# Optimization experiments

Measured on AMD Instinct MI355X. Metric: run time of the kernel, lower is better.

Reference implementation:

```python
import jax, jax.numpy as jnp
import numpy as np

B, T, C, H, E, TOPK, DR = 2, 2048, 768, 3072, 8, 2, 24


def setup_inputs() -> dict:
    key = jax.random.key(0)
    ks = jax.random.split(key, 16)
    std = 0.02
    n = lambda k, shape, s=std: (s * jax.random.normal(k, shape)).astype(jnp.float32)
    emb = jax.random.normal(ks[3], (E, DR), dtype=jnp.float32)
    emb = emb / (jnp.linalg.norm(emb, axis=-1, keepdims=True) + 1e-8)
    return {
        "x": jax.random.normal(ks[0], (B, T, C), dtype=jnp.float32),
        "router_w": n(ks[1], (E, C)),
        "probe_w": n(ks[2], (DR, C)),
        "router_emb": emb,
        "fatigue": jnp.zeros((E,), jnp.float32),
        "energy": jnp.ones((E,), jnp.float32),
        "w_fast1": n(ks[4], (E, C, H)),
        "w_slow1": n(ks[5], (E, C, H)),
        "h_fast1": n(ks[6], (E, C, H), 0.005),
        "m_gate1": jax.random.uniform(ks[7], (E,), dtype=jnp.float32),
        "b1": jnp.zeros((E, H), jnp.float32),
        "w_fast2": n(ks[8], (E, H, C)),
        "w_slow2": n(ks[9], (E, H, C)),
        "h_fast2": n(ks[10], (E, H, C), 0.005),
        "m_gate2": jax.random.uniform(ks[11], (E,), dtype=jnp.float32),
        "b2": jnp.zeros((E, C), jnp.float32),
    }


def _normalize(v, axis=-1, eps=1e-12):
    # matches F.normalize: v / max(||v||, eps)
    return v / jnp.maximum(jnp.linalg.norm(v, axis=axis, keepdims=True), eps)


def reference(x, router_w, probe_w, router_emb, fatigue, energy,
              w_fast1, w_slow1, h_fast1, m_gate1, b1,
              w_fast2, w_slow2, h_fast2, m_gate2, b2):
    Bd, Td, Cd = x.shape
    # --- router logits with biology-inspired biases ---
    logits = jnp.einsum('btc,ec->bte', x, router_w)            # nn.Linear, no bias
    tok_proxy = x.mean(axis=-1, keepdims=True)                  # [B,T,1]
    router_gain = jnp.linalg.norm(router_emb, axis=-1)          # [E]
    base_bias = 0.02 * tok_proxy                                # broadcasts over E
    gain_bias = 0.02 * tok_proxy * router_gain                  # [B,T,E]
    tok_unit = _normalize(jnp.einsum('btc,dc->btd', x, probe_w))
    align_bias = 0.02 * jnp.einsum('btd,ed->bte', tok_unit, _normalize(router_emb))
    logits = logits + base_bias + gain_bias + align_bias + 0.1 * energy - 0.1 * fatigue
    # --- top-k gating ---
    g, idx = jax.lax.top_k(logits, TOPK)                        # [B,T,K]
    gates = jax.nn.softmax(g, axis=-1)
    N = Bd * Td
    gates_full = jnp.zeros((N, E), x.dtype).at[
        jnp.arange(N)[:, None], idx.reshape(N, TOPK)].set(gates.reshape(N, TOPK))
    flat_x = x.reshape(N, Cd)
    # --- expert dispatch: dynamic W = w_fast + m_gate*w_slow + H_fast ---
    def body(acc, p):
        wf1, ws1, hf1, mg1, bb1, wf2, ws2, hf2, mg2, bb2, ge = p
        W1 = wf1 + mg1 * ws1 + hf1                              # [C,H]
        h = jnp.square(jnp.maximum(flat_x @ W1 + bb1, 0.0))     # relu(y)^2
        W2 = wf2 + mg2 * ws2 + hf2                              # [H,C]
        y = h @ W2 + bb2
        return acc + ge[:, None] * y, None
    out, _ = jax.lax.scan(
        body, jnp.zeros((N, Cd), x.dtype),
        (w_fast1, w_slow1, h_fast1, m_gate1, b1,
         w_fast2, w_slow2, h_fast2, m_gate2, b2, gates_full.T))
    return out.reshape(Bd, Td, Cd)
```

## Files before the change

kernel.cpp:

```cpp
#include <hip/hip_runtime.h>

typedef unsigned short u16;
typedef __attribute__((ext_vector_type(8))) short short8;
typedef __attribute__((ext_vector_type(8))) unsigned short ushort8;
typedef __attribute__((ext_vector_type(4))) unsigned short ushort4v;
typedef __attribute__((ext_vector_type(4))) float f32x4;

static constexpr int Cdim = 768;
static constexpr int Hdim = 3072;
static constexpr int Edim = 8;
static constexpr int Ntok = 4096;
static constexpr int DRc  = 24;
static constexpr int NSLOT = Ntok * 2;
static constexpr int NCHUNK = 8;
static constexpr int CCH = Cdim / NCHUNK;
static constexpr int KS2 = 3;
static constexpr int KC2 = Hdim / KS2;
static constexpr int MAXROWS = 71;

static constexpr size_t OFF_XB   = 0;
static constexpr size_t OFF_W1T  = 6291456;
static constexpr size_t OFF_W2T  = 44040192;
static constexpr size_t OFF_HBUF = 81788928;
static constexpr size_t OFF_XT   = OFF_HBUF;
static constexpr size_t OFF_PART = OFF_HBUF + 12582912;
static constexpr size_t OFF_YB   = OFF_W1T;
static constexpr size_t OFF_TOK  = 132120576;
static constexpr size_t OFF_RM   = 132251648;
static constexpr size_t OFF_NR   = 132252160;
static constexpr size_t OFF_CNT  = 132382720;
static constexpr size_t OFF_OFFS = 132382752;
static constexpr size_t OFF_TSLOT= 132382784;
static constexpr size_t OFF_TG   = 132448320;

__device__ __forceinline__ u16 f2bf(float f) {
  unsigned u = __builtin_bit_cast(unsigned, f);
  u += 0x7fffu + ((u >> 16) & 1u);
  return (u16)(u >> 16);
}

__device__ __forceinline__ float bf2f(u16 v) {
  unsigned u = ((unsigned)v) << 16;
  return __builtin_bit_cast(float, u);
}

__device__ __forceinline__ void gld16(const u16* g, u16* l) {
  __builtin_amdgcn_global_load_lds((const __attribute__((address_space(1))) unsigned int*)g,
                                   (__attribute__((address_space(3))) unsigned int*)l,
                                   16, 0, 0);
}

__device__ __forceinline__ int xcd_remap(int p, int nwg) {
  int q = nwg >> 3, rem = nwg & 7;
  int x = p & 7, i = p >> 3;
  return (x < rem ? x * (q + 1) : rem * (q + 1) + (x - rem) * q) + i;
}

__global__ __launch_bounds__(256)
void prep_x2_kernel(const float* __restrict__ x, u16* __restrict__ x16,
                    float* __restrict__ xT) {
  __shared__ float tile[64][65];
  const int c0 = blockIdx.x * 64;
  const int t0 = blockIdx.y * 64;
  const int tid = threadIdx.x;
  const int row = tid >> 4, col = (tid & 15) * 4;
  #pragma unroll
  for (int i = 0; i < 4; i++) {
    int r = row + i * 16;
    size_t idx = (size_t)(t0 + r) * Cdim + c0 + col;
    float4 v = *(const float4*)(x + idx);
    tile[r][col + 0] = v.x; tile[r][col + 1] = v.y;
    tile[r][col + 2] = v.z; tile[r][col + 3] = v.w;
    ushort4v o = { f2bf(v.x), f2bf(v.y), f2bf(v.z), f2bf(v.w) };
    *reinterpret_cast<ushort4v*>(x16 + idx) = o;
  }
  __syncthreads();
  const int c = tid >> 2, tg = (tid & 3) * 16;
  #pragma unroll
  for (int q = 0; q < 4; q++) {
    float4 w;
    w.x = tile[tg + q * 4 + 0][c];
    w.y = tile[tg + q * 4 + 1][c];
    w.z = tile[tg + q * 4 + 2][c];
    w.w = tile[tg + q * 4 + 3][c];
    *reinterpret_cast<float4*>(xT + (size_t)(c0 + c) * Ntok + t0 + tg + q * 4) = w;
  }
}

__global__ __launch_bounds__(256)
void prep_wt_kernel(const float* __restrict__ wf, const float* __restrict__ wsl,
                    const float* __restrict__ hf, const float* __restrict__ mg,
                    u16* __restrict__ outw, const int R, const int Ccol) {
  __shared__ u16 tileT[64][66];
  const int e = blockIdx.z;
  const int r0 = blockIdx.x * 64, c0 = blockIdx.y * 64;
  const float m = mg[e];
  const size_t base = (size_t)e * R * Ccol;
  const int t = threadIdx.x;
  const int cr = t >> 4, cc = (t & 15) * 4;
  #pragma unroll
  for (int i = 0; i < 4; i++) {
    int r = cr + i * 16;
    size_t idx = base + (size_t)(r0 + r) * Ccol + (c0 + cc);
    float4 a = *(const float4*)(wf + idx);
    float4 b = *(const float4*)(wsl + idx);
    float4 h = *(const float4*)(hf + idx);
    tileT[cc + 0][r] = f2bf(fmaf(m, b.x, a.x) + h.x);
    tileT[cc + 1][r] = f2bf(fmaf(m, b.y, a.y) + h.y);
    tileT[cc + 2][r] = f2bf(fmaf(m, b.z, a.z) + h.z);
    tileT[cc + 3][r] = f2bf(fmaf(m, b.w, a.w) + h.w);
  }
  __syncthreads();
  const int oc = t >> 2, ch = (t & 3) * 16;
  ushort8 o0, o1;
  #pragma unroll
  for (int j = 0; j < 8; j++) { o0[j] = tileT[oc][ch + j]; o1[j] = tileT[oc][ch + 8 + j]; }
  size_t oidx = ((size_t)e * Ccol + c0 + oc) * R + r0 + ch;
  *reinterpret_cast<ushort8*>(outw + oidx) = o0;
  *reinterpret_cast<ushort8*>(outw + oidx + 8) = o1;
}

__global__ __launch_bounds__(256)
void logits_part_kernel(const float* __restrict__ xT, const float* __restrict__ router_w,
                        const float* __restrict__ probe_w, float* __restrict__ part) {
  const int t = blockIdx.x * 256 + threadIdx.x;
  const int cB = blockIdx.y * CCH;
  float racc[Edim] = {};
  float pacc[DRc] = {};
  float sacc = 0.f;
  for (int ci = 0; ci < CCH; ci++) {
    int c = cB + ci;
    float xv = xT[(size_t)c * Ntok + t];
    sacc += xv;
    #pragma unroll
    for (int ee = 0; ee < Edim; ee++) racc[ee] = fmaf(xv, router_w[ee * Cdim + c], racc[ee]);
    #pragma unroll
    for (int d = 0; d < DRc; d++) pacc[d] = fmaf(xv, probe_w[d * Cdim + c], pacc[d]);
  }
  float* pb = part + (size_t)blockIdx.y * 33 * Ntok + t;
  #pragma unroll
  for (int ee = 0; ee < Edim; ee++) pb[(size_t)ee * Ntok] = racc[ee];
  #pragma unroll
  for (int d = 0; d < DRc; d++) pb[(size_t)(8 + d) * Ntok] = pacc[d];
  pb[(size_t)32 * Ntok] = sacc;
}

__global__ __launch_bounds__(256)
void router_fin_kernel(const float* __restrict__ part, const float* __restrict__ emb,
                       const float* __restrict__ fatigue, const float* __restrict__ energy,
                       int* __restrict__ counts, int* __restrict__ tok_list,
                       int4* __restrict__ tokslot, float2* __restrict__ tokgate) {
  const int t = blockIdx.x * 256 + threadIdx.x;
  float v[33];
  #pragma unroll
  for (int o = 0; o < 33; o++) {
    float s = 0.f;
    #pragma unroll
    for (int ch = 0; ch < NCHUNK; ch++)
      s += part[((size_t)ch * 33 + o) * Ntok + t];
    v[o] = s;
  }
  const float* racc = v;
  const float* pacc = v + 8;
  float proxy = v[32] / 768.f;
  float pn2 = 0.f;
  #pragma unroll
  for (int d = 0; d < DRc; d++) pn2 += pacc[d] * pacc[d];
  float pnorm = sqrtf(pn2);
  float logitv[Edim];
  #pragma unroll
  for (int ee = 0; ee < Edim; ee++) {
    float g2 = 0.f, dote = 0.f;
    #pragma unroll
    for (int d = 0; d < DRc; d++) {
      float ev = emb[ee * DRc + d];
      g2 += ev * ev;
      dote += pacc[d] * ev;
    }
    float gain = sqrtf(g2);
    float align = dote / (fmaxf(pnorm, 1e-12f) * fmaxf(gain, 1e-12f));
    logitv[ee] = racc[ee] + 0.02f * proxy * (1.f + gain) + 0.02f * align
               + 0.1f * energy[ee] - 0.1f * fatigue[ee];
  }
  int e0 = 0; float b0v = logitv[0];
  #pragma unroll
  for (int ee = 1; ee < Edim; ee++) if (logitv[ee] > b0v) { b0v = logitv[ee]; e0 = ee; }
  int e1 = -1; float b1v = -3.4e38f;
  #pragma unroll
  for (int ee = 0; ee < Edim; ee++) if (ee != e0 && logitv[ee] > b1v) { b1v = logitv[ee]; e1 = ee; }
  float texp = expf(b1v - b0v);
  float g0 = 1.f / (1.f + texp);
  float g1 = texp / (1.f + texp);
  int p0 = atomicAdd(&counts[e0], 1);
  tok_list[e0 * Ntok + p0] = t;
  int p1 = atomicAdd(&counts[e1], 1);
  tok_list[e1 * Ntok + p1] = t;
  tokslot[t] = make_int4(e0, p0, e1, p1);
  tokgate[t] = make_float2(g0, g1);
}

__global__ void offsets_kernel(const int* __restrict__ counts, int* __restrict__ offs,
                               int* __restrict__ rowmap, int* __restrict__ nrows) {
  if (threadIdx.x == 0) {
    int r = 0, nr = 0;
    for (int e = 0; e < Edim; e++) {
      offs[e] = r;
      int ne = counts[e];
      for (int tb = 0; tb < ne; tb += 128) rowmap[nr++] = (e << 16) | (tb >> 7);
      r += ne;
    }
    nrows[0] = nr;
  }
}

__global__ __launch_bounds__(256)
void fc1_kernel(const u16* __restrict__ x16, const u16* __restrict__ W1T,
                const float* __restrict__ b1, const int* __restrict__ counts,
                const int* __restrict__ offs, const int* __restrict__ tok_list,
                const int* __restrict__ rowmap, const int* __restrict__ nrows,
                u16* __restrict__ h_buf) {
  const int l = xcd_remap(blockIdx.x, MAXROWS * 24);
  const int r = l / 24;
  if (r >= nrows[0]) return;
  const int hB = l % 24;
  const int rm = rowmap[r];
  const int e = rm >> 16;
  const int tokBase = (rm & 0xffff) << 7;
  const int n_e = counts[e];
  const int hBase = hB * 128;
  __shared__ u16 As[2][4096];
  __shared__ u16 Bs[2][4096];
  __shared__ int toks[128];
  const int tid = threadIdx.x;
  if (tid < 128) {
    int s = tokBase + tid;
    toks[tid] = (s < n_e) ? tok_list[e * Ntok + s] : 0;
  }
  __syncthreads();
  const int lane = tid & 63, wv = tid >> 6;
  const int wr = wv >> 1, wc = wv & 1;
  const int sRow = lane >> 2, sSlot = lane & 3;
  const int kbOff = (sSlot ^ ((sRow >> 1) & 3)) * 8;
  const int rA0 = wv * 16 + sRow, rA1 = 64 + rA0;
  const u16* pA0 = x16 + (size_t)toks[rA0] * Cdim + kbOff;
  const u16* pA1 = x16 + (size_t)toks[rA1] * Cdim + kbOff;
  const u16* pB0 = W1T + ((size_t)e * Hdim + hBase + rA0) * Cdim + kbOff;
  const u16* pB1 = W1T + ((size_t)e * Hdim + hBase + rA1) * Cdim + kbOff;
  const int stOff = wv * 512 + lane * 8;
  const int fr = lane & 15;
  const int qsw = (((lane >> 4) ^ ((fr >> 1) & 3))) * 8;
  f32x4 acc[4][4] = {};
  gld16(pA0, &As[0][stOff]);
  gld16(pA1, &As[0][2048 + stOff]);
  gld16(pB0, &Bs[0][stOff]);
  gld16(pB1, &Bs[0][2048 + stOff]);
  __syncthreads();
  int cur = 0;
  for (int it = 0; it < 24; it++) {
    if (it < 23) {
      int k1 = (it + 1) * 32;
      gld16(pA0 + k1, &As[cur ^ 1][stOff]);
      gld16(pA1 + k1, &As[cur ^ 1][2048 + stOff]);
      gld16(pB0 + k1, &Bs[cur ^ 1][stOff]);
      gld16(pB1 + k1, &Bs[cur ^ 1][2048 + stOff]);
    }
    short8 aF[4], bF[4];
    #pragma unroll
    for (int m = 0; m < 4; m++)
      aF[m] = *reinterpret_cast<const short8*>(&As[cur][(wr * 64 + m * 16 + fr) * 32 + qsw]);
    #pragma unroll
    for (int n = 0; n < 4; n++)
      bF[n] = *reinterpret_cast<const short8*>(&Bs[cur][(wc * 64 + n * 16 + fr) * 32 + qsw]);
    #pragma unroll
    for (int m = 0; m < 4; m++)
      #pragma unroll
      for (int n = 0; n < 4; n++)
        acc[m][n] = __builtin_amdgcn_mfma_f32_16x16x32_bf16(aF[m], bF[n], acc[m][n], 0, 0, 0);
    __syncthreads();
    cur ^= 1;
  }
  const int rq = (lane >> 4) * 4;
  float bias[4];
  #pragma unroll
  for (int n = 0; n < 4; n++) bias[n] = b1[(size_t)e * Hdim + hBase + wc * 64 + n * 16 + fr];
  const int rowB = offs[e] + tokBase;
  #pragma unroll
  for (int m = 0; m < 4; m++) {
    #pragma unroll
    for (int j = 0; j < 4; j++) {
      int rl = wr * 64 + m * 16 + rq + j;
      if (tokBase + rl < n_e) {
        size_t rb = (size_t)(rowB + rl) * Hdim + hBase + wc * 64 + fr;
        #pragma unroll
        for (int n = 0; n < 4; n++) {
          float v = fmaxf(acc[m][n][j] + bias[n], 0.f);
          h_buf[rb + n * 16] = f2bf(v * v);
        }
      }
    }
  }
}

__global__ __launch_bounds__(256)
void fc2_kernel(const u16* __restrict__ h_buf, const u16* __restrict__ W2T,
                const float* __restrict__ b2, const int* __restrict__ counts,
                const int* __restrict__ offs, const int* __restrict__ rowmap,
                const int* __restrict__ nrows, u16* __restrict__ ybuf) {
  const int l = xcd_remap(blockIdx.x, MAXROWS * 18);
  const int r = l / 18;
  if (r >= nrows[0]) return;
  const int xb = l % 18;
  const int rm = rowmap[r];
  const int e = rm >> 16;
  const int tokBase = (rm & 0xffff) << 7;
  const int n_e = counts[e];
  const int kch = xb / 6;
  const int cBase = (xb % 6) * 128;
  const size_t kOff = (size_t)kch * KC2;
  __shared__ u16 As[2][4096];
  __shared__ u16 Bs[2][4096];
  const int tid = threadIdx.x;
  const int lane = tid & 63, wv = tid >> 6;
  const int wr = wv >> 1, wc = wv & 1;
  const int sRow = lane >> 2, sSlot = lane & 3;
  const int kbOff = (sSlot ^ ((sRow >> 1) & 3)) * 8;
  const int rA0 = wv * 16 + sRow, rA1 = 64 + rA0;
  const int slotB = offs[e] + tokBase;
  const int s0 = min(slotB + rA0, NSLOT - 1);
  const int s1 = min(slotB + rA1, NSLOT - 1);
  const u16* pA0 = h_buf + (size_t)s0 * Hdim + kOff + kbOff;
  const u16* pA1 = h_buf + (size_t)s1 * Hdim + kOff + kbOff;
  const u16* pB0 = W2T + ((size_t)e * Cdim + cBase + rA0) * Hdim + kOff + kbOff;
  const u16* pB1 = W2T + ((size_t)e * Cdim + cBase + rA1) * Hdim + kOff + kbOff;
  const int stOff = wv * 512 + lane * 8;
  const int fr = lane & 15;
  const int qsw = (((lane >> 4) ^ ((fr >> 1) & 3))) * 8;
  f32x4 acc[4][4] = {};
  gld16(pA0, &As[0][stOff]);
  gld16(pA1, &As[0][2048 + stOff]);
  gld16(pB0, &Bs[0][stOff]);
  gld16(pB1, &Bs[0][2048 + stOff]);
  __syncthreads();
  int cur = 0;
  for (int it = 0; it < KC2 / 32; it++) {
    if (it < KC2 / 32 - 1) {
      int k1 = (it + 1) * 32;
      gld16(pA0 + k1, &As[cur ^ 1][stOff]);
      gld16(pA1 + k1, &As[cur ^ 1][2048 + stOff]);
      gld16(pB0 + k1, &Bs[cur ^ 1][stOff]);
      gld16(pB1 + k1, &Bs[cur ^ 1][2048 + stOff]);
    }
    short8 aF[4], bF[4];
    #pragma unroll
    for (int m = 0; m < 4; m++)
      aF[m] = *reinterpret_cast<const short8*>(&As[cur][(wr * 64 + m * 16 + fr) * 32 + qsw]);
    #pragma unroll
    for (int n = 0; n < 4; n++)
      bF[n] = *reinterpret_cast<const short8*>(&Bs[cur][(wc * 64 + n * 16 + fr) * 32 + qsw]);
    #pragma unroll
    for (int m = 0; m < 4; m++)
      #pragma unroll
      for (int n = 0; n < 4; n++)
        acc[m][n] = __builtin_amdgcn_mfma_f32_16x16x32_bf16(aF[m], bF[n], acc[m][n], 0, 0, 0);
    __syncthreads();
    cur ^= 1;
  }
  const int rq = (lane >> 4) * 4;
  float bias[4];
  #pragma unroll
  for (int n = 0; n < 4; n++)
    bias[n] = (kch == 0) ? b2[(size_t)e * Cdim + cBase + wc * 64 + n * 16 + fr] : 0.f;
  u16* yb = ybuf + (size_t)kch * NSLOT * Cdim;
  #pragma unroll
  for (int m = 0; m < 4; m++) {
    #pragma unroll
    for (int j = 0; j < 4; j++) {
      int rl = wr * 64 + m * 16 + rq + j;
      if (tokBase + rl < n_e) {
        u16* ob = yb + (size_t)(slotB + rl) * Cdim + cBase + wc * 64 + fr;
        #pragma unroll
        for (int n = 0; n < 4; n++)
          ob[n * 16] = f2bf(acc[m][n][j] + bias[n]);
      }
    }
  }
}

__global__ __launch_bounds__(256)
void gather_kernel(const u16* __restrict__ ybuf, const int4* __restrict__ tokslot,
                   const float2* __restrict__ tokgate, const int* __restrict__ offs,
                   float* __restrict__ out) {
  const int gid = blockIdx.x * 256 + threadIdx.x;
  const int t = gid / 192;
  const int c4 = (gid - t * 192) * 4;
  int4 ts = tokslot[t];
  float2 g = tokgate[t];
  size_t s0 = (size_t)(offs[ts.x] + ts.y) * Cdim + c4;
  size_t s1 = (size_t)(offs[ts.z] + ts.w) * Cdim + c4;
  const size_t K1 = (size_t)NSLOT * Cdim;
  float acc0[4] = {}, acc1[4] = {};
  #pragma unroll
  for (int k = 0; k < KS2; k++) {
    ushort4v a = *reinterpret_cast<const ushort4v*>(ybuf + k * K1 + s0);
    ushort4v b = *reinterpret_cast<const ushort4v*>(ybuf + k * K1 + s1);
    #pragma unroll
    for (int j = 0; j < 4; j++) { acc0[j] += bf2f(a[j]); acc1[j] += bf2f(b[j]); }
  }
  float4 o;
  o.x = g.x * acc0[0] + g.y * acc1[0];
  o.y = g.x * acc0[1] + g.y * acc1[1];
  o.z = g.x * acc0[2] + g.y * acc1[2];
  o.w = g.x * acc0[3] + g.y * acc1[3];
  *reinterpret_cast<float4*>(out + (size_t)t * Cdim + c4) = o;
}

extern "C" void kernel_launch(void* const* d_in, const int* in_sizes, int n_in,
                              void* d_out, int out_size, void* d_ws, size_t ws_size,
                              hipStream_t stream) {
  const float* x        = (const float*)d_in[0];
  const float* router_w = (const float*)d_in[1];
  const float* probe_w  = (const float*)d_in[2];
  const float* emb      = (const float*)d_in[3];
  const float* fatigue  = (const float*)d_in[4];
  const float* energy   = (const float*)d_in[5];
  const float* wf1      = (const float*)d_in[6];
  const float* ws1      = (const float*)d_in[7];
  const float* hf1      = (const float*)d_in[8];
  const float* mg1      = (const float*)d_in[9];
  const float* b1       = (const float*)d_in[10];
  const float* wf2      = (const float*)d_in[11];
  const float* ws2      = (const float*)d_in[12];
  const float* hf2      = (const float*)d_in[13];
  const float* mg2      = (const float*)d_in[14];
  const float* b2       = (const float*)d_in[15];
  float* out = (float*)d_out;
  char* ws = (char*)d_ws;

  u16*    x16       = (u16*)(ws + OFF_XB);
  u16*    W1T       = (u16*)(ws + OFF_W1T);
  u16*    W2T       = (u16*)(ws + OFF_W2T);
  u16*    hbuf      = (u16*)(ws + OFF_HBUF);
  float*  xT        = (float*)(ws + OFF_XT);
  float*  part      = (float*)(ws + OFF_PART);
  u16*    ybuf      = (u16*)(ws + OFF_YB);
  int*    tok_list  = (int*)(ws + OFF_TOK);
  int*    rowmap    = (int*)(ws + OFF_RM);
  int*    nrows     = (int*)(ws + OFF_NR);
  int*    counts    = (int*)(ws + OFF_CNT);
  int*    offs      = (int*)(ws + OFF_OFFS);
  int4*   tokslot   = (int4*)(ws + OFF_TSLOT);
  float2* tokgate   = (float2*)(ws + OFF_TG);

  hipMemsetAsync(counts, 0, 64, stream);

  prep_x2_kernel<<<dim3(Cdim / 64, Ntok / 64), 256, 0, stream>>>(x, x16, xT);
  logits_part_kernel<<<dim3(Ntok / 256, NCHUNK), 256, 0, stream>>>(xT, router_w, probe_w, part);
  router_fin_kernel<<<Ntok / 256, 256, 0, stream>>>(part, emb, fatigue, energy,
                                                    counts, tok_list, tokslot, tokgate);
  prep_wt_kernel<<<dim3(Cdim / 64, Hdim / 64, Edim), 256, 0, stream>>>(wf1, ws1, hf1, mg1, W1T, Cdim, Hdim);
  prep_wt_kernel<<<dim3(Hdim / 64, Cdim / 64, Edim), 256, 0, stream>>>(wf2, ws2, hf2, mg2, W2T, Hdim, Cdim);
  offsets_kernel<<<1, 64, 0, stream>>>(counts, offs, rowmap, nrows);
  fc1_kernel<<<MAXROWS * 24, 256, 0, stream>>>(x16, W1T, b1, counts, offs, tok_list,
                                               rowmap, nrows, hbuf);
  fc2_kernel<<<MAXROWS * 18, 256, 0, stream>>>(hbuf, W2T, b2, counts, offs,
                                               rowmap, nrows, ybuf);
  gather_kernel<<<Ntok * 192 / 256, 256, 0, stream>>>(ybuf, tokslot, tokgate, offs, out);
  (void)in_sizes; (void)n_in; (void)out_size; (void)ws_size;
}
```

Baseline: 353.3 us.

## Merge weight prep into one wider-tile kernel and relax GEMM loop barriers

The two weight-combine-and-transpose launches become a single kernel. Each block now processes a 64x256 tile with full-row coalesced float4 reads and row-contiguous LDS writes, which cuts launch count and improves read coalescing on the roughly 226 MB weight stream. The fc1 and fc2 double-buffered loops replace __syncthreads with an explicit s_waitcnt vmcnt(4) plus a raw s_barrier, so the next tile's prefetch can stay in flight while the current tile is consumed. This relies on the per-wave vmcnt ordering of the global-to-LDS loads being correct, and the LDS transpose read pattern may introduce bank conflicts.

```diff
diff --git a/kernel.cpp b/kernel.cpp
--- a/kernel.cpp
+++ b/kernel.cpp
@@ -17,6 +17,7 @@
 static constexpr int KS2 = 3;
 static constexpr int KC2 = Hdim / KS2;
 static constexpr int MAXROWS = 71;
+static constexpr int NPREP = 2304;
 
 static constexpr size_t OFF_XB   = 0;
 static constexpr size_t OFF_W1T  = 6291456;
@@ -87,37 +88,62 @@
   }
 }
 
-__global__ __launch_bounds__(256)
-void prep_wt_kernel(const float* __restrict__ wf, const float* __restrict__ wsl,
-                    const float* __restrict__ hf, const float* __restrict__ mg,
-                    u16* __restrict__ outw, const int R, const int Ccol) {
-  __shared__ u16 tileT[64][66];
-  const int e = blockIdx.z;
-  const int r0 = blockIdx.x * 64, c0 = blockIdx.y * 64;
-  const float m = mg[e];
-  const size_t base = (size_t)e * R * Ccol;
+template<int R, int CCOL>
+__device__ __forceinline__ void prep_wt_body(const float* __restrict__ wf,
+                                             const float* __restrict__ wsl,
+                                             const float* __restrict__ hf, float m,
+                                             u16* __restrict__ outw, int e, int r0, int c0,
+                                             u16* tile) {
+  const size_t base = (size_t)e * R * CCOL;
   const int t = threadIdx.x;
-  const int cr = t >> 4, cc = (t & 15) * 4;
-  #pragma unroll
-  for (int i = 0; i < 4; i++) {
-    int r = cr + i * 16;
-    size_t idx = base + (size_t)(r0 + r) * Ccol + (c0 + cc);
+  const int lr = t >> 6;
+  const int lc = (t & 63) * 4;
+  #pragma unroll 4
+  for (int i = 0; i < 16; i++) {
+    int r = i * 4 + lr;
+    size_t idx = base + (size_t)(r0 + r) * CCOL + c0 + lc;
     float4 a = *(const float4*)(wf + idx);
     float4 b = *(const float4*)(wsl + idx);
     float4 h = *(const float4*)(hf + idx);
-    tileT[cc + 0][r] = f2bf(fmaf(m, b.x, a.x) + h.x);
-    tileT[cc + 1][r] = f2bf(fmaf(m, b.y, a.y) + h.y);
-    tileT[cc + 2][r] = f2bf(fmaf(m, b.z, a.z) + h.z);
-    tileT[cc + 3][r] = f2bf(fmaf(m, b.w, a.w) + h.w);
+    ushort4v o = { f2bf(fmaf(m, b.x, a.x) + h.x), f2bf(fmaf(m, b.y, a.y) + h.y),
+                   f2bf(fmaf(m, b.z, a.z) + h.z), f2bf(fmaf(m, b.w, a.w) + h.w) };
+    *reinterpret_cast<ushort4v*>(&tile[r * 264 + lc]) = o;
   }
   __syncthreads();
-  const int oc = t >> 2, ch = (t & 3) * 16;
-  ushort8 o0, o1;
-  #pragma unroll
-  for (int j = 0; j < 8; j++) { o0[j] = tileT[oc][ch + j]; o1[j] = tileT[oc][ch + 8 + j]; }
-  size_t oidx = ((size_t)e * Ccol + c0 + oc) * R + r0 + ch;
-  *reinterpret_cast<ushort8*>(outw + oidx) = o0;
-  *reinterpret_cast<ushort8*>(outw + oidx + 8) = o1;
+  const int oc = t >> 2;
+  const int rseg = (t & 3) * 16;
+  #pragma unroll
+  for (int cq = 0; cq < 4; cq++) {
+    int c = cq * 64 + oc;
+    ushort8 o0, o1;
+    #pragma unroll
+    for (int j = 0; j < 8; j++) {
+      o0[j] = tile[(rseg + j) * 264 + c];
+      o1[j] = tile[(rseg + 8 + j) * 264 + c];
+    }
+    size_t oidx = ((size_t)e * CCOL + c0 + c) * R + r0 + rseg;
+    *reinterpret_cast<ushort8*>(outw + oidx) = o0;
+    *reinterpret_cast<ushort8*>(outw + oidx + 8) = o1;
+  }
+}
+
+__global__ __launch_bounds__(256)
+void prep_wt2_kernel(const float* __restrict__ wf1, const float* __restrict__ ws1,
+                     const float* __restrict__ hf1, const float* __restrict__ mg1,
+                     u16* __restrict__ o1,
+                     const float* __restrict__ wf2, const float* __restrict__ ws2,
+                     const float* __restrict__ hf2, const float* __restrict__ mg2,
+                     u16* __restrict__ o2) {
+  __shared__ u16 tile[64 * 264];
+  int bid = blockIdx.x;
+  if (bid < 1152) {
+    int xx = bid % 12, yy = (bid / 12) % 12, e = bid / 144;
+    prep_wt_body<768, 3072>(wf1, ws1, hf1, mg1[e], o1, e, xx * 64, yy * 256, tile);
+  } else {
+    bid -= 1152;
+    int xx = bid % 48, yy = (bid / 48) % 3, e = bid / 144;
+    prep_wt_body<3072, 768>(wf2, ws2, hf2, mg2[e], o2, e, xx * 64, yy * 256, tile);
+  }
 }
 
 __global__ __launch_bounds__(256)
@@ -254,7 +280,8 @@
   gld16(pA1, &As[0][2048 + stOff]);
   gld16(pB0, &Bs[0][stOff]);
   gld16(pB1, &Bs[0][2048 + stOff]);
-  __syncthreads();
+  asm volatile("s_waitcnt vmcnt(0)" ::: "memory");
+  __builtin_amdgcn_s_barrier();
   int cur = 0;
   for (int it = 0; it < 24; it++) {
     if (it < 23) {
@@ -263,7 +290,11 @@
       gld16(pA1 + k1, &As[cur ^ 1][2048 + stOff]);
       gld16(pB0 + k1, &Bs[cur ^ 1][stOff]);
       gld16(pB1 + k1, &Bs[cur ^ 1][2048 + stOff]);
-    }
+      asm volatile("s_waitcnt vmcnt(4)" ::: "memory");
+    } else {
+      asm volatile("s_waitcnt vmcnt(0)" ::: "memory");
+    }
+    __builtin_amdgcn_s_barrier();
     short8 aF[4], bF[4];
     #pragma unroll
     for (int m = 0; m < 4; m++)
@@ -276,7 +307,7 @@
       #pragma unroll
       for (int n = 0; n < 4; n++)
         acc[m][n] = __builtin_amdgcn_mfma_f32_16x16x32_bf16(aF[m], bF[n], acc[m][n], 0, 0, 0);
-    __syncthreads();
+    __builtin_amdgcn_s_barrier();
     cur ^= 1;
   }
   const int rq = (lane >> 4) * 4;
@@ -340,7 +371,8 @@
   gld16(pA1, &As[0][2048 + stOff]);
   gld16(pB0, &Bs[0][stOff]);
   gld16(pB1, &Bs[0][2048 + stOff]);
-  __syncthreads();
+  asm volatile("s_waitcnt vmcnt(0)" ::: "memory");
+  __builtin_amdgcn_s_barrier();
   int cur = 0;
   for (int it = 0; it < KC2 / 32; it++) {
     if (it < KC2 / 32 - 1) {
@@ -349,7 +381,11 @@
       gld16(pA1 + k1, &As[cur ^ 1][2048 + stOff]);
       gld16(pB0 + k1, &Bs[cur ^ 1][stOff]);
       gld16(pB1 + k1, &Bs[cur ^ 1][2048 + stOff]);
-    }
+      asm volatile("s_waitcnt vmcnt(4)" ::: "memory");
+    } else {
+      asm volatile("s_waitcnt vmcnt(0)" ::: "memory");
+    }
+    __builtin_amdgcn_s_barrier();
     short8 aF[4], bF[4];
     #pragma unroll
     for (int m = 0; m < 4; m++)
@@ -362,7 +398,7 @@
       #pragma unroll
       for (int n = 0; n < 4; n++)
         acc[m][n] = __builtin_amdgcn_mfma_f32_16x16x32_bf16(aF[m], bF[n], acc[m][n], 0, 0, 0);
-    __syncthreads();
+    __builtin_amdgcn_s_barrier();
     cur ^= 1;
   }
   const int rq = (lane >> 4) * 4;
@@ -457,8 +493,8 @@
   logits_part_kernel<<<dim3(Ntok / 256, NCHUNK), 256, 0, stream>>>(xT, router_w, probe_w, part);
   router_fin_kernel<<<Ntok / 256, 256, 0, stream>>>(part, emb, fatigue, energy,
                                                     counts, tok_list, tokslot, tokgate);
-  prep_wt_kernel<<<dim3(Cdim / 64, Hdim / 64, Edim), 256, 0, stream>>>(wf1, ws1, hf1, mg1, W1T, Cdim, Hdim);
-  prep_wt_kernel<<<dim3(Hdim / 64, Cdim / 64, Edim), 256, 0, stream>>>(wf2, ws2, hf2, mg2, W2T, Hdim, Cdim);
+  prep_wt2_kernel<<<NPREP, 256, 0, stream>>>(wf1, ws1, hf1, mg1, W1T,
+                                             wf2, ws2, hf2, mg2, W2T);
   offsets_kernel<<<1, 64, 0, stream>>>(counts, offs, rowmap, nrows);
   fc1_kernel<<<MAXROWS * 24, 256, 0, stream>>>(x16, W1T, b1, counts, offs, tok_list,
                                                rowmap, nrows, hbuf);
```

Measured after the change: 355.4 us. No clear change (+0.6%).
